# Optimization experiments

Hardware: AMD Instinct MI355X
Metric: run time of the kernel (lower is better)

Reference implementation:

```python
import jax, jax.numpy as jnp
import numpy as np

B, L, H, HEADS, BLOCKS, TSPAN = 8, 256, 256, 4, 2, 512
D = H // HEADS
BIG_NEG = jnp.float32(-2.0**32 + 1)


def _layernorm(x, g, b, eps=1e-8):
    m = x.mean(-1, keepdims=True)
    v = ((x - m) ** 2).mean(-1, keepdims=True)
    return (x - m) / jnp.sqrt(v + eps) * g + b


def _forward(seq_emb, Wq, bq, Wk, bk, Wv, bv, ln1_g, ln1_b, ln2_g, ln2_b,
             W1, b1, W2, b2, pos_K, pos_V, tK_emb, tV_emb, lnf_g, lnf_b,
             mask, time_matrices):
    # relative time-interval embeddings: [B,L,L,H] -> per-head [B,L,L,heads,D]
    tmKh = tK_emb[time_matrices].reshape(B, L, L, HEADS, D)
    tmVh = tV_emb[time_matrices].reshape(B, L, L, HEADS, D)
    posKh = pos_K.reshape(L, HEADS, D)  # abs position embs (positions = arange(L))
    posVh = pos_V.reshape(L, HEADS, D)
    keep = (~mask)[..., None].astype(seq_emb.dtype)  # [B,L,1], True mask = pad
    causal = ~jnp.tril(jnp.ones((L, L), dtype=bool))  # True above diagonal
    x = seq_emb * keep
    scale = jnp.sqrt(jnp.float32(D))
    for i in range(BLOCKS):
        q = _layernorm(x, ln1_g[i], ln1_b[i])  # queries normalized, keys/values raw
        Qh = (q @ Wq[i].T + bq[i]).reshape(B, L, HEADS, D)
        Kh = (x @ Wk[i].T + bk[i]).reshape(B, L, HEADS, D)
        Vh = (x @ Wv[i].T + bv[i]).reshape(B, L, HEADS, D)
        aw = (jnp.einsum('bqhd,bkhd->bhqk', Qh, Kh)
              + jnp.einsum('bqhd,khd->bhqk', Qh, posKh)
              + jnp.einsum('bqhd,bqkhd->bhqk', Qh, tmKh)) / scale
        aw = jnp.where(mask[:, None, :, None] | causal[None, None], BIG_NEG, aw)
        p = jax.nn.softmax(aw, axis=-1)
        out = (jnp.einsum('bhqk,bkhd->bqhd', p, Vh)
               + jnp.einsum('bhqk,khd->bqhd', p, posVh)
               + jnp.einsum('bhqk,bqkhd->bqhd', p, tmVh)).reshape(B, L, H)
        x = q + out
        x = _layernorm(x, ln2_g[i], ln2_b[i])
        h = jax.nn.relu(jnp.einsum('bld,od->blo', x, W1[i]) + b1[i])  # Conv1d k=1 == Linear
        x = jnp.einsum('bld,od->blo', h, W2[i]) + b2[i] + x
        x = x * keep
    return _layernorm(x, lnf_g, lnf_b)


def setup_inputs():
    key = jax.random.key(0)
    ks = jax.random.split(key, 24)
    s = 0.02
    nrm = lambda k, shape: jax.random.normal(k, shape, dtype=jnp.float32) * s
    inp = {}
    inp['mask'] = jax.random.uniform(ks[0], (B, L)) < 0.1
    inp['seq_emb'] = jax.random.normal(ks[1], (B, L, H), dtype=jnp.float32)
    inp['log_seqs'] = jax.random.randint(ks[2], (B, L), 0, 1000)
    inp['time_matrices'] = jax.random.randint(ks[3], (B, L, L), 0, TSPAN + 1).astype(jnp.int32)
    inp['time_attn'] = 0
    inp['Wq'] = nrm(ks[4], (BLOCKS, H, H)); inp['bq'] = jnp.zeros((BLOCKS, H), jnp.float32)
    inp['Wk'] = nrm(ks[5], (BLOCKS, H, H)); inp['bk'] = jnp.zeros((BLOCKS, H), jnp.float32)
    inp['Wv'] = nrm(ks[6], (BLOCKS, H, H)); inp['bv'] = jnp.zeros((BLOCKS, H), jnp.float32)
    inp['ln1_g'] = jnp.ones((BLOCKS, H), jnp.float32); inp['ln1_b'] = jnp.zeros((BLOCKS, H), jnp.float32)
    inp['ln2_g'] = jnp.ones((BLOCKS, H), jnp.float32); inp['ln2_b'] = jnp.zeros((BLOCKS, H), jnp.float32)
    inp['W1'] = nrm(ks[7], (BLOCKS, H, H)); inp['b1'] = jnp.zeros((BLOCKS, H), jnp.float32)
    inp['W2'] = nrm(ks[8], (BLOCKS, H, H)); inp['b2'] = jnp.zeros((BLOCKS, H), jnp.float32)
    inp['pos_K'] = nrm(ks[9], (L, H)); inp['pos_V'] = nrm(ks[10], (L, H))
    inp['tK_emb'] = nrm(ks[11], (TSPAN + 1, H)); inp['tV_emb'] = nrm(ks[12], (TSPAN + 1, H))
    inp['lnf_g'] = jnp.ones((H,), jnp.float32); inp['lnf_b'] = jnp.zeros((H,), jnp.float32)
    return inp


def reference(mask, seq_emb, log_seqs, time_matrices, time_attn,
              Wq, bq, Wk, bk, Wv, bv, ln1_g, ln1_b, ln2_g, ln2_b,
              W1, b1, W2, b2, pos_K, pos_V, tK_emb, tV_emb, lnf_g, lnf_b):
    return _forward(seq_emb, Wq, bq, Wk, bk, Wv, bv, ln1_g, ln1_b, ln2_g, ln2_b,
                    W1, b1, W2, b2, pos_K, pos_V, tK_emb, tV_emb, lnf_g, lnf_b,
                    mask, time_matrices)
```

## Files before the change

### kernel.cpp

```cpp
#include <hip/hip_runtime.h>

#define BIG_NEG_F (-4294967296.0f)

typedef __attribute__((ext_vector_type(8))) short bf16x8;
typedef __attribute__((ext_vector_type(4))) float f32x4;

__device__ __forceinline__ float wave_sum(float v) {
#pragma unroll
    for (int m = 32; m; m >>= 1) v += __shfl_xor(v, m, 64);
    return v;
}
__device__ __forceinline__ float wave_max(float v) {
#pragma unroll
    for (int m = 32; m; m >>= 1) v = fmaxf(v, __shfl_xor(v, m, 64));
    return v;
}

__device__ __forceinline__ unsigned int pack2(float a, float b) {
    return (__float_as_uint(b) & 0xffff0000u) | (__float_as_uint(a) >> 16);
}
__device__ __forceinline__ float hipart(float x) {
    return __uint_as_float(__float_as_uint(x) & 0xffff0000u);
}
__device__ __forceinline__ void split1(float v, unsigned short* hp, unsigned short* lp) {
    unsigned int hu = __float_as_uint(v) & 0xffff0000u;
    *hp = (unsigned short)(hu >> 16);
    *lp = (unsigned short)(__float_as_uint(v - __uint_as_float(hu)) >> 16);
}

__global__ __launch_bounds__(256) void prep_ln_kernel(const float* __restrict__ seq,
                                                      const unsigned char* __restrict__ mraw,
                                                      unsigned char* __restrict__ mout,
                                                      float* __restrict__ X, float* __restrict__ Q,
                                                      const float* __restrict__ g,
                                                      const float* __restrict__ be,
                                                      unsigned short* __restrict__ Xh,
                                                      unsigned short* __restrict__ Xl,
                                                      unsigned short* __restrict__ Qh,
                                                      unsigned short* __restrict__ Ql) {
    __shared__ int flags[2];
    __shared__ float ws[8];
    int row = blockIdx.x, tid = threadIdx.x;
    if (tid == 0) { flags[0] = 0; flags[1] = 0; }
    __syncthreads();
    for (int i = tid; i < 2048; i += 256) {
        if (mraw[i]) {
            if (i & 3) atomicOr(&flags[0], 1);
            else if (i & 4) atomicOr(&flags[1], 1);
        }
    }
    __syncthreads();
    int mode = flags[0] ? 0 : (flags[1] ? 1 : 2);
    unsigned char mrow = (mode == 0) ? mraw[row] : (mode == 1) ? mraw[row * 4] : mraw[row * 8];
    if (tid == 0) mout[row] = mrow ? 1 : 0;
    int idx = row * 256 + tid;
    int w = tid >> 6, lane = tid & 63;
    float v = mrow ? 0.f : seq[idx];
    X[idx] = v;
    split1(v, &Xh[idx], &Xl[idx]);
    float s = wave_sum(v);
    if (lane == 0) ws[w] = s;
    __syncthreads();
    float mean = (ws[0] + ws[1] + ws[2] + ws[3]) * (1.f / 256.f);
    float d = v - mean;
    float s2 = wave_sum(d * d);
    if (lane == 0) ws[4 + w] = s2;
    __syncthreads();
    float var = (ws[4] + ws[5] + ws[6] + ws[7]) * (1.f / 256.f);
    float qv = d / sqrtf(var + 1e-8f) * g[tid] + be[tid];
    Q[idx] = qv;
    split1(qv, &Qh[idx], &Ql[idx]);
}

__global__ __launch_bounds__(256) void ln_kernel(const float* __restrict__ X, float* __restrict__ Y,
                                                 const float* __restrict__ g,
                                                 const float* __restrict__ be,
                                                 unsigned short* __restrict__ Yh,
                                                 unsigned short* __restrict__ Yl) {
    __shared__ float ws[8];
    int row = blockIdx.x, tid = threadIdx.x;
    int idx = row * 256 + tid;
    int w = tid >> 6, lane = tid & 63;
    float v = X[idx];
    float s = wave_sum(v);
    if (lane == 0) ws[w] = s;
    __syncthreads();
    float mean = (ws[0] + ws[1] + ws[2] + ws[3]) * (1.f / 256.f);
    float d = v - mean;
    float s2 = wave_sum(d * d);
    if (lane == 0) ws[4 + w] = s2;
    __syncthreads();
    float var = (ws[4] + ws[5] + ws[6] + ws[7]) * (1.f / 256.f);
    float yv = d / sqrtf(var + 1e-8f) * g[tid] + be[tid];
    Y[idx] = yv;
    if (Yh) split1(yv, &Yh[idx], &Yl[idx]);
}

struct SplitJob { const float* src; unsigned short* h; unsigned short* l; };

__global__ __launch_bounds__(256) void splitw_kernel(SplitJob s0, SplitJob s1, SplitJob s2,
                                                     SplitJob s3, SplitJob s4) {
    SplitJob S = (blockIdx.z == 0) ? s0 : (blockIdx.z == 1) ? s1 : (blockIdx.z == 2) ? s2
               : (blockIdx.z == 3) ? s3 : s4;
    int i = (blockIdx.x * 256 + threadIdx.x) * 4;
    float4 v = *(const float4*)(S.src + i);
    uint2 h, l;
    h.x = pack2(v.x, v.y); h.y = pack2(v.z, v.w);
    l.x = pack2(v.x - hipart(v.x), v.y - hipart(v.y));
    l.y = pack2(v.z - hipart(v.z), v.w - hipart(v.w));
    *(uint2*)(S.h + i) = h;
    *(uint2*)(S.l + i) = l;
}

struct GemmJob {
    const unsigned short* Ah;
    const unsigned short* Al;
    const unsigned short* Wh;
    const unsigned short* Wl;
    const float* bias;
    const float* pos;
    const float* res;
    const unsigned char* maskm;
    float* C;
    unsigned short* Ch;
    unsigned short* Cl;
    int relu;
};

__global__ __launch_bounds__(256) void gemm_frag_kernel(GemmJob j0, GemmJob j1, GemmJob j2) {
    GemmJob J = (blockIdx.z == 0) ? j0 : (blockIdx.z == 1 ? j1 : j2);
    int tid = threadIdx.x, w = tid >> 6, lane = tid & 63;
    int n0 = blockIdx.x * 16;
    int m0 = blockIdx.y * 64 + w * 16;
    int r15 = lane & 15, kq = (lane >> 4) * 8;
    const unsigned short* Arh = J.Ah + (m0 + r15) * 256 + kq;
    const unsigned short* Arl = J.Al + (m0 + r15) * 256 + kq;
    const unsigned short* Brh = J.Wh + (n0 + r15) * 256 + kq;
    const unsigned short* Brl = J.Wl + (n0 + r15) * 256 + kq;
    f32x4 acc = {0.f, 0.f, 0.f, 0.f};
#pragma unroll
    for (int k = 0; k < 256; k += 32) {
        bf16x8 ah = *(const bf16x8*)(Arh + k);
        bf16x8 al = *(const bf16x8*)(Arl + k);
        bf16x8 bh = *(const bf16x8*)(Brh + k);
        bf16x8 bl = *(const bf16x8*)(Brl + k);
        acc = __builtin_amdgcn_mfma_f32_16x16x32_bf16(ah, bh, acc, 0, 0, 0);
        acc = __builtin_amdgcn_mfma_f32_16x16x32_bf16(ah, bl, acc, 0, 0, 0);
        acc = __builtin_amdgcn_mfma_f32_16x16x32_bf16(al, bh, acc, 0, 0, 0);
    }
    int col = n0 + r15;
    float bcol = J.bias[col];
    int rowb = m0 + (lane >> 4) * 4;
#pragma unroll
    for (int rr = 0; rr < 4; ++rr) {
        int m = rowb + rr;
        float v = acc[rr] + bcol;
        if (J.pos) v += J.pos[(m & 255) * 256 + col];
        if (J.relu) v = fmaxf(v, 0.f);
        if (J.res) v += J.res[m * 256 + col];
        if (J.maskm && J.maskm[m]) v = 0.f;
        J.C[m * 256 + col] = v;
        if (J.Ch) split1(v, &J.Ch[m * 256 + col], &J.Cl[m * 256 + col]);
    }
}

__global__ __launch_bounds__(256, 8) void attn_kernel(
    const float* __restrict__ Q, const float* __restrict__ Kp, const float* __restrict__ Vp,
    const float* __restrict__ qres, const int* __restrict__ tm,
    const float* __restrict__ tK, const float* __restrict__ tV,
    const float* __restrict__ g2, const float* __restrict__ b2,
    float* __restrict__ X2, unsigned short* __restrict__ X2h,
    unsigned short* __restrict__ X2l) {
    int bid = (int)blockIdx.x;
    int b = bid & 7;
    int i6 = bid >> 3;
    int jj6 = i6 & 31, a6 = i6 >> 5;
    int q0m = jj6 * 4 + (a6 >> 1);
    int qpos = (a6 & 1) ? q0m : 255 - q0m;
    int tid = threadIdx.x, w = tid >> 6, lane = tid & 63;
    __shared__ float qrow[256];
    __shared__ int   stm[256];
    __shared__ float p[4][264];
    __shared__ float opart[4][256];
    __shared__ float denom[4];
    __shared__ float lnws[8];

    int rowbase = (b * 256 + qpos) * 256;
    qrow[tid] = Q[rowbase + tid];
    {
        int t = tm[rowbase + tid];
        stm[tid] = t < 0 ? 0 : (t > 512 ? 512 : t);
    }
    __syncthreads();

    {
        int h = lane >> 4;
        const float* qr = qrow + lane * 4;
        float q0 = qr[0], q1 = qr[1], q2 = qr[2], q3 = qr[3];
        const float* Kb  = Kp + (size_t)(b << 8) * 256 + lane * 4;
        const float* tKb = tK + lane * 4;
        int nact = (qpos >= w) ? ((qpos - w) >> 2) + 1 : 0;
        int i = 0;
        for (; i + 2 <= nact; i += 2) {
            int k0 = w + 4 * i;
            float4 kv0 = *(const float4*)(Kb + (k0    ) * 256);
            float4 kv1 = *(const float4*)(Kb + (k0 + 4) * 256);
            float4 t0 = *(const float4*)(tKb + stm[k0    ] * 256);
            float4 t1 = *(const float4*)(tKb + stm[k0 + 4] * 256);
            float s0 = q0 * (kv0.x + t0.x) + q1 * (kv0.y + t0.y) + q2 * (kv0.z + t0.z) + q3 * (kv0.w + t0.w);
            float s1 = q0 * (kv1.x + t1.x) + q1 * (kv1.y + t1.y) + q2 * (kv1.z + t1.z) + q3 * (kv1.w + t1.w);
            s0 += __shfl_xor(s0, 1, 64); s1 += __shfl_xor(s1, 1, 64);
            s0 += __shfl_xor(s0, 2, 64); s1 += __shfl_xor(s1, 2, 64);
            s0 += __shfl_xor(s0, 4, 64); s1 += __shfl_xor(s1, 4, 64);
            s0 += __shfl_xor(s0, 8, 64); s1 += __shfl_xor(s1, 8, 64);
            if ((lane & 15) == 0) {
                p[h][k0    ] = s0 * 0.125f;
                p[h][k0 + 4] = s1 * 0.125f;
            }
        }
        if (i < nact) {
            int k = w + 4 * i;
            float4 kv = *(const float4*)(Kb + k * 256);
            float4 t4 = *(const float4*)(tKb + stm[k] * 256);
            float s = q0 * (kv.x + t4.x) + q1 * (kv.y + t4.y) + q2 * (kv.z + t4.z) + q3 * (kv.w + t4.w);
            s += __shfl_xor(s, 1, 64);
            s += __shfl_xor(s, 2, 64);
            s += __shfl_xor(s, 4, 64);
            s += __shfl_xor(s, 8, 64);
            if ((lane & 15) == 0) p[h][k] = s * 0.125f;
        }
    }
    __syncthreads();

    {
        float* ph = &p[w][0];
        float v0 = (lane       <= qpos) ? ph[lane      ] : BIG_NEG_F;
        float v1 = (lane + 64  <= qpos) ? ph[lane + 64 ] : BIG_NEG_F;
        float v2 = (lane + 128 <= qpos) ? ph[lane + 128] : BIG_NEG_F;
        float v3 = (lane + 192 <= qpos) ? ph[lane + 192] : BIG_NEG_F;
        float mx = wave_max(fmaxf(fmaxf(v0, v1), fmaxf(v2, v3)));
        float e0 = __expf(v0 - mx), e1 = __expf(v1 - mx), e2 = __expf(v2 - mx), e3 = __expf(v3 - mx);
        ph[lane] = e0; ph[lane + 64] = e1; ph[lane + 128] = e2; ph[lane + 192] = e3;
        float ssum = wave_sum(e0 + e1 + e2 + e3);
        if (lane == 0) denom[w] = ssum;
    }
    __syncthreads();

    {
        int hh = lane >> 4;
        const float* Vb  = Vp + (size_t)(b << 8) * 256 + lane * 4;
        const float* tVb = tV + lane * 4;
        const float* prow = &p[hh][0];
        float4 a0 = {0.f, 0.f, 0.f, 0.f}, a1 = a0;
        int cnt = (qpos >= w) ? ((qpos - w) >> 2) + 1 : 0;
        int i = 0;
        for (; i + 2 <= cnt; i += 2) {
            int k0 = w + 4 * i;
            float p0 = prow[k0], p1 = prow[k0 + 4];
            float4 v0 = *(const float4*)(Vb + (k0    ) * 256);
            float4 v1 = *(const float4*)(Vb + (k0 + 4) * 256);
            float4 u0 = *(const float4*)(tVb + stm[k0    ] * 256);
            float4 u1 = *(const float4*)(tVb + stm[k0 + 4] * 256);
            a0.x += p0 * (v0.x + u0.x); a0.y += p0 * (v0.y + u0.y); a0.z += p0 * (v0.z + u0.z); a0.w += p0 * (v0.w + u0.w);
            a1.x += p1 * (v1.x + u1.x); a1.y += p1 * (v1.y + u1.y); a1.z += p1 * (v1.z + u1.z); a1.w += p1 * (v1.w + u1.w);
        }
        if (i < cnt) {
            int k2 = w + 4 * i;
            float pk = prow[k2];
            float4 v = *(const float4*)(Vb + k2 * 256);
            float4 t = *(const float4*)(tVb + stm[k2] * 256);
            a0.x += pk * (v.x + t.x);
            a0.y += pk * (v.y + t.y);
            a0.z += pk * (v.z + t.z);
            a0.w += pk * (v.w + t.w);
        }
        float4 o;
        o.x = a0.x + a1.x;
        o.y = a0.y + a1.y;
        o.z = a0.z + a1.z;
        o.w = a0.w + a1.w;
        *(float4*)&opart[w][lane * 4] = o;
    }
    __syncthreads();

    {
        int d = tid, h = tid >> 6;
        float tot = opart[0][d] + opart[1][d] + opart[2][d] + opart[3][d];
        float xv = qres[rowbase + d] + tot / denom[h];
        float s = wave_sum(xv);
        if (lane == 0) lnws[w] = s;
        __syncthreads();
        float mean = (lnws[0] + lnws[1] + lnws[2] + lnws[3]) * (1.f / 256.f);
        float dd = xv - mean;
        float s2 = wave_sum(dd * dd);
        if (lane == 0) lnws[4 + w] = s2;
        __syncthreads();
        float var = (lnws[4] + lnws[5] + lnws[6] + lnws[7]) * (1.f / 256.f);
        float outv = dd / sqrtf(var + 1e-8f) * g2[d] + b2[d];
        X2[rowbase + d] = outv;
        split1(outv, &X2h[rowbase + d], &X2l[rowbase + d]);
    }
}

extern "C" void kernel_launch(void* const* d_in, const int* in_sizes, int n_in,
                              void* d_out, int out_size, void* d_ws, size_t ws_size,
                              hipStream_t stream) {
    const unsigned char* mask_raw = (const unsigned char*)d_in[0];
    const float* seq  = (const float*)d_in[1];
    const int*   tm   = (const int*)d_in[3];
    const float* Wq   = (const float*)d_in[5];
    const float* bq   = (const float*)d_in[6];
    const float* Wk   = (const float*)d_in[7];
    const float* bk   = (const float*)d_in[8];
    const float* Wv   = (const float*)d_in[9];
    const float* bv   = (const float*)d_in[10];
    const float* ln1g = (const float*)d_in[11];
    const float* ln1b = (const float*)d_in[12];
    const float* ln2g = (const float*)d_in[13];
    const float* ln2b = (const float*)d_in[14];
    const float* W1   = (const float*)d_in[15];
    const float* b1   = (const float*)d_in[16];
    const float* W2   = (const float*)d_in[17];
    const float* b2   = (const float*)d_in[18];
    const float* posK = (const float*)d_in[19];
    const float* posV = (const float*)d_in[20];
    const float* tK   = (const float*)d_in[21];
    const float* tV   = (const float*)d_in[22];
    const float* lnfg = (const float*)d_in[23];
    const float* lnfb = (const float*)d_in[24];

    const int NEL = 8 * 256 * 256;
    const int WEL = 2 * 256 * 256;
    float* x   = (float*)d_ws;
    float* q   = x   + NEL;
    float* Qb  = q   + NEL;
    float* KpB = Qb  + NEL;
    float* VpB = KpB + NEL;
    float* x2  = VpB + NEL;
    float* hb  = x2  + NEL;
    unsigned char* mask = (unsigned char*)(hb + NEL);
    unsigned short* us = (unsigned short*)(mask + 2048);
    unsigned short* qh  = us;            unsigned short* ql  = qh  + NEL;
    unsigned short* xh  = ql  + NEL;     unsigned short* xl  = xh  + NEL;
    unsigned short* x2h = xl  + NEL;     unsigned short* x2l = x2h + NEL;
    unsigned short* hbh = x2l + NEL;     unsigned short* hbl = hbh + NEL;
    unsigned short* wsp = hbl + NEL;
    unsigned short* WqH = wsp;           unsigned short* WqL = WqH + WEL;
    unsigned short* WkH = WqL + WEL;     unsigned short* WkL = WkH + WEL;
    unsigned short* WvH = WkL + WEL;     unsigned short* WvL = WvH + WEL;
    unsigned short* W1H = WvL + WEL;     unsigned short* W1L = W1H + WEL;
    unsigned short* W2H = W1L + WEL;     unsigned short* W2L = W2H + WEL;

    dim3 gSplit(128, 1, 5);
    dim3 gQKV(16, 32, 3);
    dim3 gFFN(16, 32, 1);

    SplitJob sq = {Wq, WqH, WqL}, sk = {Wk, WkH, WkL}, sv = {Wv, WvH, WvL};
    SplitJob s1 = {W1, W1H, W1L}, s2 = {W2, W2H, W2L};
    splitw_kernel<<<gSplit, 256, 0, stream>>>(sq, sk, sv, s1, s2);
    prep_ln_kernel<<<2048, 256, 0, stream>>>(seq, mask_raw, mask, x, q, ln1g, ln1b,
                                             xh, xl, qh, ql);
    for (int blk = 0; blk < 2; ++blk) {
        int o1 = blk * 256, oW = blk * 256 * 256;
        GemmJob jq = {qh, ql, WqH + oW, WqL + oW, bq + o1, nullptr, nullptr, nullptr,
                      Qb, nullptr, nullptr, 0};
        GemmJob jk = {xh, xl, WkH + oW, WkL + oW, bk + o1, posK, nullptr, nullptr,
                      KpB, nullptr, nullptr, 0};
        GemmJob jv = {xh, xl, WvH + oW, WvL + oW, bv + o1, posV, nullptr, nullptr,
                      VpB, nullptr, nullptr, 0};
        gemm_frag_kernel<<<gQKV, 256, 0, stream>>>(jq, jk, jv);
        attn_kernel<<<2048, 256, 0, stream>>>(Qb, KpB, VpB, q, tm, tK, tV,
                                              ln2g + o1, ln2b + o1, x2, x2h, x2l);
        GemmJob f1 = {x2h, x2l, W1H + oW, W1L + oW, b1 + o1, nullptr, nullptr, nullptr,
                      hb, hbh, hbl, 1};
        gemm_frag_kernel<<<gFFN, 256, 0, stream>>>(f1, f1, f1);
        GemmJob f2 = {hbh, hbl, W2H + oW, W2L + oW, b2 + o1, nullptr, x2, mask,
                      x, xh, xl, 0};
        gemm_frag_kernel<<<gFFN, 256, 0, stream>>>(f2, f2, f2);
        if (blk == 0) ln_kernel<<<2048, 256, 0, stream>>>(x, q, ln1g + 256, ln1b + 256,
                                                          qh, ql);
    }
    ln_kernel<<<2048, 256, 0, stream>>>(x, (float*)d_out, lnfg, lnfb, nullptr, nullptr);
}
```

Before: 284.0 us.

## Tile GEMM through LDS with 64x64 blocks and register-prefetched K slices

Replaces the per-wave direct-from-global 16x16 MFMA GEMM with a 64x64 block tile. Each K slice of the split-bf16 A and W operands is staged in padded shared memory, and every wave computes a 2x2 grid of 16x16 fragments. The next K slice is loaded into registers while MFMAs run on the current one. This cuts redundant global loads of A and W across blocks, at the cost of fewer blocks (a quarter of the previous grid) and extra barriers.

```diff
diff --git a/kernel.cpp b/kernel.cpp
--- a/kernel.cpp
+++ b/kernel.cpp
@@ -127,40 +127,83 @@
     int relu;
 };
 
-__global__ __launch_bounds__(256) void gemm_frag_kernel(GemmJob j0, GemmJob j1, GemmJob j2) {
+__global__ __launch_bounds__(256) void gemm_mfma_kernel(GemmJob j0, GemmJob j1, GemmJob j2) {
     GemmJob J = (blockIdx.z == 0) ? j0 : (blockIdx.z == 1 ? j1 : j2);
-    int tid = threadIdx.x, w = tid >> 6, lane = tid & 63;
-    int n0 = blockIdx.x * 16;
-    int m0 = blockIdx.y * 64 + w * 16;
-    int r15 = lane & 15, kq = (lane >> 4) * 8;
-    const unsigned short* Arh = J.Ah + (m0 + r15) * 256 + kq;
-    const unsigned short* Arl = J.Al + (m0 + r15) * 256 + kq;
-    const unsigned short* Brh = J.Wh + (n0 + r15) * 256 + kq;
-    const unsigned short* Brl = J.Wl + (n0 + r15) * 256 + kq;
-    f32x4 acc = {0.f, 0.f, 0.f, 0.f};
-#pragma unroll
-    for (int k = 0; k < 256; k += 32) {
-        bf16x8 ah = *(const bf16x8*)(Arh + k);
-        bf16x8 al = *(const bf16x8*)(Arl + k);
-        bf16x8 bh = *(const bf16x8*)(Brh + k);
-        bf16x8 bl = *(const bf16x8*)(Brl + k);
-        acc = __builtin_amdgcn_mfma_f32_16x16x32_bf16(ah, bh, acc, 0, 0, 0);
-        acc = __builtin_amdgcn_mfma_f32_16x16x32_bf16(ah, bl, acc, 0, 0, 0);
-        acc = __builtin_amdgcn_mfma_f32_16x16x32_bf16(al, bh, acc, 0, 0, 0);
-    }
-    int col = n0 + r15;
-    float bcol = J.bias[col];
-    int rowb = m0 + (lane >> 4) * 4;
-#pragma unroll
-    for (int rr = 0; rr < 4; ++rr) {
-        int m = rowb + rr;
-        float v = acc[rr] + bcol;
-        if (J.pos) v += J.pos[(m & 255) * 256 + col];
-        if (J.relu) v = fmaxf(v, 0.f);
-        if (J.res) v += J.res[m * 256 + col];
-        if (J.maskm && J.maskm[m]) v = 0.f;
-        J.C[m * 256 + col] = v;
-        if (J.Ch) split1(v, &J.Ch[m * 256 + col], &J.Cl[m * 256 + col]);
+    __shared__ unsigned short Ah[64][72], Al[64][72], Wh[64][72], Wl[64][72];
+    int tid = threadIdx.x;
+    int n0 = blockIdx.x * 64, m0 = blockIdx.y * 64;
+    int w = tid >> 6, lane = tid & 63;
+    int wm = w >> 1, wn = w & 1;
+    int srow = tid >> 2, sq = tid & 3;
+    const unsigned short* Asrc_h = J.Ah + (m0 + srow) * 256 + sq * 16;
+    const unsigned short* Asrc_l = J.Al + (m0 + srow) * 256 + sq * 16;
+    const unsigned short* Wsrc_h = J.Wh + (n0 + srow) * 256 + sq * 16;
+    const unsigned short* Wsrc_l = J.Wl + (n0 + srow) * 256 + sq * 16;
+    uint4 ah0 = *(const uint4*)(Asrc_h), ah1 = *(const uint4*)(Asrc_h + 8);
+    uint4 al0 = *(const uint4*)(Asrc_l), al1 = *(const uint4*)(Asrc_l + 8);
+    uint4 wh0 = *(const uint4*)(Wsrc_h), wh1 = *(const uint4*)(Wsrc_h + 8);
+    uint4 wl0 = *(const uint4*)(Wsrc_l), wl1 = *(const uint4*)(Wsrc_l + 8);
+    f32x4 acc[2][2] = {};
+    int r15 = lane & 15, hgrp = (lane >> 4) << 3;
+    for (int kt = 0; kt < 4; ++kt) {
+        if (kt) __syncthreads();
+        *(uint4*)&Ah[srow][sq * 16]     = ah0;  *(uint4*)&Ah[srow][sq * 16 + 8] = ah1;
+        *(uint4*)&Al[srow][sq * 16]     = al0;  *(uint4*)&Al[srow][sq * 16 + 8] = al1;
+        *(uint4*)&Wh[srow][sq * 16]     = wh0;  *(uint4*)&Wh[srow][sq * 16 + 8] = wh1;
+        *(uint4*)&Wl[srow][sq * 16]     = wl0;  *(uint4*)&Wl[srow][sq * 16 + 8] = wl1;
+        __syncthreads();
+        if (kt < 3) {
+            int ko = (kt + 1) * 64;
+            ah0 = *(const uint4*)(Asrc_h + ko); ah1 = *(const uint4*)(Asrc_h + ko + 8);
+            al0 = *(const uint4*)(Asrc_l + ko); al1 = *(const uint4*)(Asrc_l + ko + 8);
+            wh0 = *(const uint4*)(Wsrc_h + ko); wh1 = *(const uint4*)(Wsrc_h + ko + 8);
+            wl0 = *(const uint4*)(Wsrc_l + ko); wl1 = *(const uint4*)(Wsrc_l + ko + 8);
+        }
+#pragma unroll
+        for (int s = 0; s < 2; ++s) {
+            int ko = s * 32 + hgrp;
+            bf16x8 fah0 = *(const bf16x8*)&Ah[wm * 32 + r15][ko];
+            bf16x8 fah1 = *(const bf16x8*)&Ah[wm * 32 + 16 + r15][ko];
+            bf16x8 fal0 = *(const bf16x8*)&Al[wm * 32 + r15][ko];
+            bf16x8 fal1 = *(const bf16x8*)&Al[wm * 32 + 16 + r15][ko];
+            bf16x8 fbh0 = *(const bf16x8*)&Wh[wn * 32 + r15][ko];
+            bf16x8 fbh1 = *(const bf16x8*)&Wh[wn * 32 + 16 + r15][ko];
+            bf16x8 fbl0 = *(const bf16x8*)&Wl[wn * 32 + r15][ko];
+            bf16x8 fbl1 = *(const bf16x8*)&Wl[wn * 32 + 16 + r15][ko];
+            acc[0][0] = __builtin_amdgcn_mfma_f32_16x16x32_bf16(fah0, fbh0, acc[0][0], 0, 0, 0);
+            acc[0][0] = __builtin_amdgcn_mfma_f32_16x16x32_bf16(fah0, fbl0, acc[0][0], 0, 0, 0);
+            acc[0][0] = __builtin_amdgcn_mfma_f32_16x16x32_bf16(fal0, fbh0, acc[0][0], 0, 0, 0);
+            acc[0][1] = __builtin_amdgcn_mfma_f32_16x16x32_bf16(fah0, fbh1, acc[0][1], 0, 0, 0);
+            acc[0][1] = __builtin_amdgcn_mfma_f32_16x16x32_bf16(fah0, fbl1, acc[0][1], 0, 0, 0);
+            acc[0][1] = __builtin_amdgcn_mfma_f32_16x16x32_bf16(fal0, fbh1, acc[0][1], 0, 0, 0);
+            acc[1][0] = __builtin_amdgcn_mfma_f32_16x16x32_bf16(fah1, fbh0, acc[1][0], 0, 0, 0);
+            acc[1][0] = __builtin_amdgcn_mfma_f32_16x16x32_bf16(fah1, fbl0, acc[1][0], 0, 0, 0);
+            acc[1][0] = __builtin_amdgcn_mfma_f32_16x16x32_bf16(fal1, fbh0, acc[1][0], 0, 0, 0);
+            acc[1][1] = __builtin_amdgcn_mfma_f32_16x16x32_bf16(fah1, fbh1, acc[1][1], 0, 0, 0);
+            acc[1][1] = __builtin_amdgcn_mfma_f32_16x16x32_bf16(fah1, fbl1, acc[1][1], 0, 0, 0);
+            acc[1][1] = __builtin_amdgcn_mfma_f32_16x16x32_bf16(fal1, fbh1, acc[1][1], 0, 0, 0);
+        }
+    }
+#pragma unroll
+    for (int mf = 0; mf < 2; ++mf) {
+#pragma unroll
+        for (int nf = 0; nf < 2; ++nf) {
+            int col = n0 + wn * 32 + nf * 16 + r15;
+            int rowb = m0 + wm * 32 + mf * 16 + ((lane >> 4) << 2);
+            float bcol = J.bias[col];
+            f32x4 a = acc[mf][nf];
+#pragma unroll
+            for (int rr = 0; rr < 4; ++rr) {
+                int m = rowb + rr;
+                float v = a[rr] + bcol;
+                if (J.pos) v += J.pos[(m & 255) * 256 + col];
+                if (J.relu) v = fmaxf(v, 0.f);
+                if (J.res) v += J.res[m * 256 + col];
+                if (J.maskm && J.maskm[m]) v = 0.f;
+                J.C[m * 256 + col] = v;
+                if (J.Ch) split1(v, &J.Ch[m * 256 + col], &J.Cl[m * 256 + col]);
+            }
+        }
     }
 }
 
@@ -352,8 +395,8 @@
     unsigned short* W2H = W1L + WEL;     unsigned short* W2L = W2H + WEL;
 
     dim3 gSplit(128, 1, 5);
-    dim3 gQKV(16, 32, 3);
-    dim3 gFFN(16, 32, 1);
+    dim3 gQKV(4, 32, 3);
+    dim3 gFFN(4, 32, 1);
 
     SplitJob sq = {Wq, WqH, WqL}, sk = {Wk, WkH, WkL}, sv = {Wv, WvH, WvL};
     SplitJob s1 = {W1, W1H, W1L}, s2 = {W2, W2H, W2L};
@@ -368,15 +411,15 @@
                       KpB, nullptr, nullptr, 0};
         GemmJob jv = {xh, xl, WvH + oW, WvL + oW, bv + o1, posV, nullptr, nullptr,
                       VpB, nullptr, nullptr, 0};
-        gemm_frag_kernel<<<gQKV, 256, 0, stream>>>(jq, jk, jv);
+        gemm_mfma_kernel<<<gQKV, 256, 0, stream>>>(jq, jk, jv);
         attn_kernel<<<2048, 256, 0, stream>>>(Qb, KpB, VpB, q, tm, tK, tV,
                                               ln2g + o1, ln2b + o1, x2, x2h, x2l);
         GemmJob f1 = {x2h, x2l, W1H + oW, W1L + oW, b1 + o1, nullptr, nullptr, nullptr,
                       hb, hbh, hbl, 1};
-        gemm_frag_kernel<<<gFFN, 256, 0, stream>>>(f1, f1, f1);
+        gemm_mfma_kernel<<<gFFN, 256, 0, stream>>>(f1, f1, f1);
         GemmJob f2 = {hbh, hbl, W2H + oW, W2L + oW, b2 + o1, nullptr, x2, mask,
                       x, xh, xl, 0};
-        gemm_frag_kernel<<<gFFN, 256, 0, stream>>>(f2, f2, f2);
+        gemm_mfma_kernel<<<gFFN, 256, 0, stream>>>(f2, f2, f2);
         if (blk == 0) ln_kernel<<<2048, 256, 0, stream>>>(x, q, ln1g + 256, ln1b + 256,
                                                           qh, ql);
     }
```

After: 257.8 us. 9.2% less time.
